# Kernel tuning notes

Hardware: AMD Instinct MI355X
Metric: run time of the kernel (lower is better)

The kernel has to match this reference:

```python
import jax, jax.numpy as jnp
import numpy as np

B, T, C, H = 8, 512, 1024, 16
N = C // H
DW, DA, DG = 64, 64, 128  # LoRA dims for decay / icl-rate / gate at C=1024

def _ln(x, w, b, eps=1e-5):
    mu = x.mean(-1, keepdims=True)
    var = ((x - mu) ** 2).mean(-1, keepdims=True)
    return (x - mu) * jax.lax.rsqrt(var + eps) * w + b

def _gn_heads(x, w, b, eps=64e-5):
    # GroupNorm(H groups) over channel dim of (B,T,C)
    xh = x.reshape(x.shape[0], x.shape[1], H, N)
    mu = xh.mean(-1, keepdims=True)
    var = ((xh - mu) ** 2).mean(-1, keepdims=True)
    xh = (xh - mu) * jax.lax.rsqrt(var + eps)
    return xh.reshape(x.shape) * w + b

def _shift(x):
    # RWKV time_shift: ZeroPad2d((0,0,1,-1))
    return jnp.concatenate([jnp.zeros_like(x[:, :1]), x[:, :-1]], axis=1)

def _wkv7(r, w_log, k, v, a, b):
    # all (B,T,H,N); state S (B,H,N,N): S = S*diag(exp(-exp(w))) + (S@a)b^T + v k^T; out = S@r
    decay = jnp.exp(-jnp.exp(w_log))
    def step(state, inp):
        r_t, d_t, k_t, v_t, a_t, b_t = inp
        sa = jnp.einsum('bhij,bhj->bhi', state, a_t)
        state = (state * d_t[:, :, None, :]
                 + sa[..., None] * b_t[:, :, None, :]
                 + v_t[..., None] * k_t[:, :, None, :])
        return state, jnp.einsum('bhij,bhj->bhi', state, r_t)
    xs = tuple(jnp.moveaxis(t, 1, 0) for t in (r, decay, k, v, a, b))
    s0 = jnp.zeros((r.shape[0], H, N, N), r.dtype)
    _, out = jax.lax.scan(step, s0, xs)
    return jnp.moveaxis(out, 0, 1)

def reference(x, v_first, ln_pre_w, ln_pre_b, ln_attn_w, ln_attn_b, ln_ffn_w, ln_ffn_b,
              x_r, x_w, x_k, x_v, x_a, x_g, w0, w1, w2, a0, a1, a2, g1, g2,
              k_k, k_a, r_k, W_r, W_k, W_v, W_o, gn_w, gn_b,
              ffn_x_k, W_ffn1, W_ffn2):
    Bx, Tx = x.shape[0], x.shape[1]
    x = _ln(x, ln_pre_w, ln_pre_b)            # pre_norm (layer_idx==0)
    # --- time mixing (RWKV7Attention) ---
    xn = _ln(x, ln_attn_w, ln_attn_b)
    dx = _shift(xn) - xn
    xr = xn + dx * x_r; xw = xn + dx * x_w; xk = xn + dx * x_k
    xv = xn + dx * x_v; xa = xn + dx * x_a; xg = xn + dx * x_g
    r = xr @ W_r
    w_log = -jax.nn.softplus(-(w0 + jnp.tanh(xw @ w1) @ w2)) - 0.5
    k = xk @ W_k
    v = xv @ W_v
    v_first = v                               # layer 0 stores v
    a = jax.nn.sigmoid(a0 + (xa @ a1) @ a2)   # in-context learning rate
    g = jax.nn.sigmoid(xg @ g1) @ g2          # gate
    kk = (k * k_k).reshape(Bx, Tx, H, N)
    kk = kk / jnp.maximum(jnp.linalg.norm(kk, axis=-1, keepdims=True), 1e-12)
    k = k * (1.0 + (a - 1.0) * k_a)
    rh = r.reshape(Bx, Tx, H, N)
    kh = k.reshape(Bx, Tx, H, N)
    vh = v.reshape(Bx, Tx, H, N)
    ah = a.reshape(Bx, Tx, H, N)
    o = _wkv7(rh, w_log.reshape(Bx, Tx, H, N), kh, vh, -kk, kk * ah)
    o = _gn_heads(o.reshape(Bx, Tx, C), gn_w, gn_b)
    o = o + ((rh * kh * r_k).sum(-1, keepdims=True) * vh).reshape(Bx, Tx, C)
    x = x + (o * g) @ W_o                     # residual (dropout p=0)
    # --- channel mixing (RWKV7FeedForward) ---
    xf = _ln(x, ln_ffn_w, ln_ffn_b)
    kf = xf + (_shift(xf) - xf) * ffn_x_k
    x = x + jnp.square(jax.nn.relu(kf @ W_ffn1)) @ W_ffn2
    return x, v_first

def setup_inputs() -> dict:
    key = jax.random.key(0)
    ks = iter(jax.random.split(key, 40))
    def nrm(shape, s=0.02):
        return jax.random.normal(next(ks), shape, jnp.float32) * s
    f32 = jnp.float32
    d = {
        'x': jax.random.normal(next(ks), (B, T, C), f32),
        'v_first': jnp.zeros((B, T, C), f32),
        'ln_pre_w': jnp.ones((C,), f32), 'ln_pre_b': jnp.zeros((C,), f32),
        'ln_attn_w': jnp.ones((C,), f32), 'ln_attn_b': jnp.zeros((C,), f32),
        'ln_ffn_w': jnp.ones((C,), f32), 'ln_ffn_b': jnp.zeros((C,), f32),
        'x_r': nrm((C,), 0.1), 'x_w': nrm((C,), 0.1), 'x_k': nrm((C,), 0.1),
        'x_v': nrm((C,), 0.1), 'x_a': nrm((C,), 0.1), 'x_g': nrm((C,), 0.1),
        'w0': nrm((C,), 0.5), 'w1': nrm((C, DW)), 'w2': nrm((DW, C)),
        'a0': nrm((C,), 0.1), 'a1': nrm((C, DA)), 'a2': nrm((DA, C)),
        'g1': nrm((C, DG)), 'g2': nrm((DG, C)),
        'k_k': 0.85 * jnp.ones((C,), f32) + nrm((C,), 0.05),
        'k_a': jnp.ones((C,), f32),
        'r_k': nrm((H, N), 0.1),
        'W_r': nrm((C, C)), 'W_k': nrm((C, C)), 'W_v': nrm((C, C)), 'W_o': nrm((C, C)),
        'gn_w': jnp.ones((C,), f32), 'gn_b': jnp.zeros((C,), f32),
        'ffn_x_k': nrm((C,), 0.1),
        'W_ffn1': nrm((C, 4 * C)), 'W_ffn2': nrm((4 * C, C)),
    }
    return d
```

## Files before the change

kernel.cpp:

```cpp
#include <hip/hip_runtime.h>

#define Bb 8
#define Tt 512
#define Cc 1024
#define Hh 16
#define Nh 64
#define Mm 4096
#define BTC 4194304
#define DEV __device__ __forceinline__

typedef __attribute__((ext_vector_type(8))) short short8;
typedef __attribute__((ext_vector_type(4))) float f32x4;

DEV unsigned short f2bf(float f) {
  unsigned int u = __builtin_bit_cast(unsigned int, f);
  u += 0x7fffu + ((u >> 16) & 1u);
  return (unsigned short)(u >> 16);
}

template <int CTRL>
DEV float dppadd(float x) {
  int xi = __builtin_bit_cast(int, x);
  int yi = __builtin_amdgcn_update_dpp(0, xi, CTRL, 0xF, 0xF, true);
  return x + __builtin_bit_cast(float, yi);
}

struct TDesc { const float* in; unsigned short* out; int K, N, bstart, nbx; };
struct TPack { TDesc d[12]; };

__global__ __launch_bounds__(256) void kt_transpose_multi(TPack p) {
  __shared__ float tile[32][33];
  const int bid = blockIdx.x;
  int i = 0;
  #pragma unroll
  for (int j = 1; j < 12; ++j) if (bid >= p.d[j].bstart) i = j;
  const float* in = p.d[i].in;
  unsigned short* out = p.d[i].out;
  const int K = p.d[i].K, N = p.d[i].N;
  const int local = bid - p.d[i].bstart;
  const int byq = local / p.d[i].nbx;
  const int bx = (local - byq * p.d[i].nbx) * 32;
  const int by = byq * 32;
  int tx = threadIdx.x, ty = threadIdx.y;
  #pragma unroll
  for (int q = ty; q < 32; q += 8) {
    int kk = by + q, nn = bx + tx;
    tile[q][tx] = (kk < K && nn < N) ? in[(size_t)kk * N + nn] : 0.f;
  }
  __syncthreads();
  #pragma unroll
  for (int q = ty; q < 32; q += 8) {
    int nn = bx + q, kk = by + tx;
    if (nn < N && kk < K) out[(size_t)nn * K + kk] = f2bf(tile[tx][q]);
  }
}

DEV void row_stats(float v0, float v1, float v2, float v3, float* red,
                   float& mu, float& rs, float eps) {
  float s = v0 + v1 + v2 + v3;
  float q = v0 * v0 + v1 * v1 + v2 * v2 + v3 * v3;
  #pragma unroll
  for (int o = 32; o; o >>= 1) { s += __shfl_down(s, o); q += __shfl_down(q, o); }
  int w = threadIdx.x >> 6;
  __syncthreads();
  if ((threadIdx.x & 63) == 0) { red[w] = s; red[4 + w] = q; }
  __syncthreads();
  s = red[0] + red[1] + red[2] + red[3];
  q = red[4] + red[5] + red[6] + red[7];
  mu = s * (1.f / 1024.f);
  float var = q * (1.f / 1024.f) - mu * mu;
  rs = rsqrtf(var + eps);
}

__global__ __launch_bounds__(256) void k1_mix(
    const float* __restrict__ x,
    const float* __restrict__ lnpw, const float* __restrict__ lnpb,
    const float* __restrict__ lnaw, const float* __restrict__ lnab,
    const float* __restrict__ cr, const float* __restrict__ cw,
    const float* __restrict__ ck, const float* __restrict__ cv,
    const float* __restrict__ ca, const float* __restrict__ cg,
    float* __restrict__ xln,
    unsigned short* __restrict__ mR, unsigned short* __restrict__ mW,
    unsigned short* __restrict__ mK, unsigned short* __restrict__ mV,
    unsigned short* __restrict__ mA, unsigned short* __restrict__ mG) {
  __shared__ float red[8];
  const int row = blockIdx.x;
  const int t = row & (Tt - 1);
  const int tid = threadIdx.x;
  const int c = tid * 4;
  const size_t base = (size_t)row * Cc + c;
  float a0 = x[base], a1 = x[base + 1], a2 = x[base + 2], a3 = x[base + 3];
  float mu, rs;
  row_stats(a0, a1, a2, a3, red, mu, rs, 1e-5f);
  float pw0 = lnpw[c], pw1 = lnpw[c + 1], pw2 = lnpw[c + 2], pw3 = lnpw[c + 3];
  float pb0 = lnpb[c], pb1 = lnpb[c + 1], pb2 = lnpb[c + 2], pb3 = lnpb[c + 3];
  float l0 = (a0 - mu) * rs * pw0 + pb0, l1 = (a1 - mu) * rs * pw1 + pb1;
  float l2 = (a2 - mu) * rs * pw2 + pb2, l3 = (a3 - mu) * rs * pw3 + pb3;
  float4 st; st.x = l0; st.y = l1; st.z = l2; st.w = l3;
  *(float4*)(xln + base) = st;
  row_stats(l0, l1, l2, l3, red, mu, rs, 1e-5f);
  float aw0 = lnaw[c], aw1 = lnaw[c + 1], aw2 = lnaw[c + 2], aw3 = lnaw[c + 3];
  float ab0 = lnab[c], ab1 = lnab[c + 1], ab2 = lnab[c + 2], ab3 = lnab[c + 3];
  float n0 = (l0 - mu) * rs * aw0 + ab0, n1 = (l1 - mu) * rs * aw1 + ab1;
  float n2 = (l2 - mu) * rs * aw2 + ab2, n3 = (l3 - mu) * rs * aw3 + ab3;
  float p0 = 0.f, p1 = 0.f, p2 = 0.f, p3 = 0.f;
  if (t > 0) {
    const size_t pb_ = base - Cc;
    float q0 = x[pb_], q1 = x[pb_ + 1], q2 = x[pb_ + 2], q3 = x[pb_ + 3];
    row_stats(q0, q1, q2, q3, red, mu, rs, 1e-5f);
    float e0 = (q0 - mu) * rs * pw0 + pb0, e1 = (q1 - mu) * rs * pw1 + pb1;
    float e2 = (q2 - mu) * rs * pw2 + pb2, e3 = (q3 - mu) * rs * pw3 + pb3;
    row_stats(e0, e1, e2, e3, red, mu, rs, 1e-5f);
    p0 = (e0 - mu) * rs * aw0 + ab0; p1 = (e1 - mu) * rs * aw1 + ab1;
    p2 = (e2 - mu) * rs * aw2 + ab2; p3 = (e3 - mu) * rs * aw3 + ab3;
  }
  float d0 = p0 - n0, d1 = p1 - n1, d2 = p2 - n2, d3 = p3 - n3;
  #define EMIT(cf, dst) { \
    float f0 = cf[c], f1 = cf[c + 1], f2 = cf[c + 2], f3 = cf[c + 3]; \
    ushort4 u; u.x = f2bf(n0 + d0 * f0); u.y = f2bf(n1 + d1 * f1); \
    u.z = f2bf(n2 + d2 * f2); u.w = f2bf(n3 + d3 * f3); \
    *(ushort4*)(dst + base) = u; }
  EMIT(cr, mR) EMIT(cw, mW) EMIT(ck, mK) EMIT(cv, mV) EMIT(ca, mA) EMIT(cg, mG)
  #undef EMIT
}

DEV void gll16(const unsigned short* g, unsigned short* l) {
  __builtin_amdgcn_global_load_lds(
      (const __attribute__((address_space(1))) void*)g,
      (__attribute__((address_space(3))) void*)l, 16, 0, 0);
}

template <int MODE>
DEV void gemm_epi(float z, size_t oi, int col,
                  float* outF, unsigned short* outB,
                  const float* bias, const float* res, float* outF2) {
  if constexpr (MODE == 0) outF[oi] = z;
  else if constexpr (MODE == 1) outB[oi] = f2bf(z);
  else if constexpr (MODE == 2) outB[oi] = f2bf(tanhf(z));
  else if constexpr (MODE == 3) outB[oi] = f2bf(1.f / (1.f + expf(-z)));
  else if constexpr (MODE == 4) { float m = fmaxf(z, 0.f); outB[oi] = f2bf(m * m); }
  else if constexpr (MODE == 5) { z += bias[col]; outF[oi] = 1.f / (1.f + expf(-z)); }
  else if constexpr (MODE == 6) {
    z += bias[col];
    float sg = 1.f / (1.f + expf(-z));
    outF[oi] = expf(-0.6065306597126334f * sg);
  } else if constexpr (MODE == 7) { outF[oi] = z + res[oi]; }
  else { float v = z + res[oi]; outF[oi] = v; outF2[oi] = v; }
}

DEV void gemm_epi_rt(int mode, float z, size_t oi, int col,
                     float* outF, unsigned short* outB, const float* bias) {
  if (mode == 0) outF[oi] = z;
  else if (mode == 1) outB[oi] = f2bf(z);
  else if (mode == 2) outB[oi] = f2bf(tanhf(z));
  else if (mode == 3) outB[oi] = f2bf(1.f / (1.f + expf(-z)));
  else if (mode == 5) { z += bias[col]; outF[oi] = 1.f / (1.f + expf(-z)); }
  else { z += bias[col]; float sg = 1.f / (1.f + expf(-z));
         outF[oi] = expf(-0.6065306597126334f * sg); }
}

template <int MODE>
__global__ __launch_bounds__(256) void kg_gemm64(
    const unsigned short* __restrict__ A, const unsigned short* __restrict__ Bt,
    int M, int Nn, int K,
    float* __restrict__ outF, unsigned short* __restrict__ outB,
    const float* __restrict__ bias, const float* __restrict__ res,
    float* __restrict__ outF2) {
  __shared__ unsigned short lsA[128 * 32];
  __shared__ unsigned short lsB[64 * 32];
  const int tid = threadIdx.x;
  const int lane = tid & 63;
  const int wave = tid >> 6;
  const int wy = wave >> 1, wx = wave & 1;
  const int m0 = blockIdx.y * 128;
  const int n0 = blockIdx.x * 64;
  const int sl4 = lane >> 2;
  const int sc = (lane & 3) << 3;
  f32x4 acc[4][2];
  #pragma unroll
  for (int i = 0; i < 4; ++i)
    #pragma unroll
    for (int j = 0; j < 2; ++j) { f32x4 z = {0.f, 0.f, 0.f, 0.f}; acc[i][j] = z; }
  const int fr = lane & 15;
  const int fk = (lane >> 4) << 3;
  for (int k0 = 0; k0 < K; k0 += 32) {
    #pragma unroll
    for (int j = 0; j < 2; ++j) {
      const int rb = (wave + j * 4) * 16;
      gll16(A + (size_t)(m0 + rb + sl4) * K + k0 + sc, lsA + rb * 32);
    }
    {
      const int rb = wave * 16;
      int br = n0 + rb + sl4;
      br = br < Nn ? br : Nn - 1;
      gll16(Bt + (size_t)br * K + k0 + sc, lsB + rb * 32);
    }
    __syncthreads();
    short8 af[4], bf[2];
    #pragma unroll
    for (int mt = 0; mt < 4; ++mt)
      af[mt] = *(const short8*)(lsA + (wy * 64 + mt * 16 + fr) * 32 + fk);
    #pragma unroll
    for (int nt = 0; nt < 2; ++nt)
      bf[nt] = *(const short8*)(lsB + (wx * 32 + nt * 16 + fr) * 32 + fk);
    #pragma unroll
    for (int mt = 0; mt < 4; ++mt)
      #pragma unroll
      for (int nt = 0; nt < 2; ++nt)
        acc[mt][nt] = __builtin_amdgcn_mfma_f32_16x16x32_bf16(af[mt], bf[nt], acc[mt][nt], 0, 0, 0);
    __syncthreads();
  }
  const int rbase = (lane >> 4) << 2;
  const int cbase = lane & 15;
  #pragma unroll
  for (int mt = 0; mt < 4; ++mt)
    #pragma unroll
    for (int nt = 0; nt < 2; ++nt)
      #pragma unroll
      for (int rr = 0; rr < 4; ++rr) {
        int row = m0 + wy * 64 + mt * 16 + rbase + rr;
        int col = n0 + wx * 32 + nt * 16 + cbase;
        if (col < Nn)
          gemm_epi<MODE>(acc[mt][nt][rr], (size_t)row * Nn + col, col, outF, outB, bias, res, outF2);
      }
}

DEV void gemm_body_rt(const unsigned short* A, const unsigned short* Bt,
                      int Nn, int K,
                      float* outF, unsigned short* outB, const float* bias,
                      unsigned short* lsA, unsigned short* lsB,
                      int m0, int n0, int mode) {
  const int tid = threadIdx.x;
  const int lane = tid & 63;
  const int wave = tid >> 6;
  const int wy = wave >> 1, wx = wave & 1;
  const int sl4 = lane >> 2;
  const int sc = (lane & 3) << 3;
  f32x4 acc[4][2];
  #pragma unroll
  for (int i = 0; i < 4; ++i)
    #pragma unroll
    for (int j = 0; j < 2; ++j) { f32x4 z = {0.f, 0.f, 0.f, 0.f}; acc[i][j] = z; }
  const int fr = lane & 15;
  const int fk = (lane >> 4) << 3;
  for (int k0 = 0; k0 < K; k0 += 32) {
    #pragma unroll
    for (int j = 0; j < 2; ++j) {
      const int rb = (wave + j * 4) * 16;
      gll16(A + (size_t)(m0 + rb + sl4) * K + k0 + sc, lsA + rb * 32);
    }
    {
      const int rb = wave * 16;
      int br = n0 + rb + sl4;
      br = br < Nn ? br : Nn - 1;
      gll16(Bt + (size_t)br * K + k0 + sc, lsB + rb * 32);
    }
    __syncthreads();
    short8 af[4], bf[2];
    #pragma unroll
    for (int mt = 0; mt < 4; ++mt)
      af[mt] = *(const short8*)(lsA + (wy * 64 + mt * 16 + fr) * 32 + fk);
    #pragma unroll
    for (int nt = 0; nt < 2; ++nt)
      bf[nt] = *(const short8*)(lsB + (wx * 32 + nt * 16 + fr) * 32 + fk);
    #pragma unroll
    for (int mt = 0; mt < 4; ++mt)
      #pragma unroll
      for (int nt = 0; nt < 2; ++nt)
        acc[mt][nt] = __builtin_amdgcn_mfma_f32_16x16x32_bf16(af[mt], bf[nt], acc[mt][nt], 0, 0, 0);
    __syncthreads();
  }
  const int rbase = (lane >> 4) << 2;
  const int cbase = lane & 15;
  #pragma unroll
  for (int mt = 0; mt < 4; ++mt)
    #pragma unroll
    for (int nt = 0; nt < 2; ++nt)
      #pragma unroll
      for (int rr = 0; rr < 4; ++rr) {
        int row = m0 + wy * 64 + mt * 16 + rbase + rr;
        int col = n0 + wx * 32 + nt * 16 + cbase;
        if (col < Nn)
          gemm_epi_rt(mode, acc[mt][nt][rr], (size_t)row * Nn + col, col, outF, outB, bias);
      }
}

__global__ __launch_bounds__(256) void kg_lora1(
    const unsigned short* __restrict__ mW, const unsigned short* __restrict__ mA,
    const unsigned short* __restrict__ mG,
    const unsigned short* __restrict__ w1T, const unsigned short* __restrict__ a1T,
    const unsigned short* __restrict__ g1T,
    unsigned short* __restrict__ tmpw, unsigned short* __restrict__ tmpa,
    unsigned short* __restrict__ tmpg) {
  __shared__ unsigned short lsA[128 * 32];
  __shared__ unsigned short lsB[64 * 32];
  const int z = blockIdx.z;
  const unsigned short* A  = z == 0 ? mW : z == 1 ? mA : mG;
  const unsigned short* Bt = z == 0 ? w1T : z == 1 ? a1T : g1T;
  unsigned short* outB     = z == 0 ? tmpw : z == 1 ? tmpa : tmpg;
  const int Nn = z < 2 ? 64 : 128;
  const int n0 = z < 2 ? 0 : (z - 2) * 64;
  const int mode = z == 0 ? 2 : z == 1 ? 1 : 3;
  gemm_body_rt(A, Bt, Nn, 1024, nullptr, outB, nullptr, lsA, lsB,
               blockIdx.y * 128, n0, mode);
}

__global__ __launch_bounds__(256) void kg_lora2(
    const unsigned short* __restrict__ tmpw, const unsigned short* __restrict__ tmpa,
    const unsigned short* __restrict__ tmpg,
    const unsigned short* __restrict__ w2T, const unsigned short* __restrict__ a2T,
    const unsigned short* __restrict__ g2T,
    float* __restrict__ decay, float* __restrict__ aicl, float* __restrict__ gout,
    const float* __restrict__ w0v, const float* __restrict__ a0v) {
  __shared__ unsigned short lsA[128 * 32];
  __shared__ unsigned short lsB[64 * 32];
  const int z = blockIdx.z;
  const unsigned short* A  = z == 0 ? tmpw : z == 1 ? tmpa : tmpg;
  const unsigned short* Bt = z == 0 ? w2T : z == 1 ? a2T : g2T;
  float* outF              = z == 0 ? decay : z == 1 ? aicl : gout;
  const float* bias        = z == 0 ? w0v : z == 1 ? a0v : nullptr;
  const int K = z < 2 ? 64 : 128;
  const int mode = z == 0 ? 6 : z == 1 ? 5 : 0;
  gemm_body_rt(A, Bt, 1024, K, outF, nullptr, bias, lsA, lsB,
               blockIdx.y * 128, blockIdx.x * 64, mode);
}

template <int MODE>
__global__ __launch_bounds__(512, 1) void kg_gemm8p(
    const unsigned short* __restrict__ A, const unsigned short* __restrict__ Bt,
    int Nn, int Kstride, int Klen,
    float* __restrict__ outF, unsigned short* __restrict__ outB) {
  __shared__ unsigned short lds[3 * 24576];
  const int tid = threadIdx.x;
  const int lane = tid & 63;
  const int wave = tid >> 6;
  const int wm = wave >> 2, wn = wave & 3;
  const int m0 = blockIdx.y * 128;
  const int n0 = blockIdx.x * 256;
  const int kbase = blockIdx.z * Klen;
  const int ntile = Klen / 64;
  const int fr = lane & 15;
  const int fkb = (lane >> 4) << 4;

  int arow[2], acolb[2], brow[4], bcolb[4];
  #pragma unroll
  for (int i = 0; i < 2; ++i) {
    int off = i * 8192 + tid * 16;
    int r = off >> 7;
    arow[i] = r; acolb[i] = (off & 127) ^ ((r & 7) << 4);
  }
  #pragma unroll
  for (int i = 0; i < 4; ++i) {
    int off = i * 8192 + tid * 16;
    int r = off >> 7;
    brow[i] = r; bcolb[i] = (off & 127) ^ ((r & 7) << 4);
  }

  #define STAGE(t_) { \
    int tc = (t_) < ntile ? (t_) : ntile - 1; \
    unsigned short* lb_ = lds + ((t_) % 3) * 24576; \
    const int kk = kbase + tc * 64; \
    _Pragma("unroll") \
    for (int i = 0; i < 2; ++i) \
      gll16(A + (size_t)(m0 + arow[i]) * Kstride + kk + (acolb[i] >> 1), \
            lb_ + i * 4096 + wave * 512); \
    _Pragma("unroll") \
    for (int i = 0; i < 4; ++i) \
      gll16(Bt + (size_t)(n0 + brow[i]) * Kstride + kk + (bcolb[i] >> 1), \
            lb_ + 8192 + i * 4096 + wave * 512); \
  }

  f32x4 acc[4][4];
  #pragma unroll
  for (int i = 0; i < 4; ++i)
    #pragma unroll
    for (int j = 0; j < 4; ++j) { f32x4 z = {0.f, 0.f, 0.f, 0.f}; acc[i][j] = z; }

  STAGE(0)
  STAGE(1)
  asm volatile("s_waitcnt vmcnt(6)" ::: "memory");
  __syncthreads();

  for (int t = 0; t < ntile; ++t) {
    STAGE(t + 2)
    const unsigned short* lb = lds + (t % 3) * 24576;
    #pragma unroll
    for (int ks = 0; ks < 2; ++ks) {
      short8 af[4], bf[4];
      #pragma unroll
      for (int mt = 0; mt < 4; ++mt) {
        int r = wm * 64 + mt * 16 + fr;
        int byt = (ks * 64 + fkb) ^ ((r & 7) << 4);
        af[mt] = *(const short8*)(lb + r * 64 + (byt >> 1));
      }
      #pragma unroll
      for (int nt = 0; nt < 4; ++nt) {
        int r = wn * 64 + nt * 16 + fr;
        int byt = (ks * 64 + fkb) ^ ((r & 7) << 4);
        bf[nt] = *(const short8*)(lb + 8192 + r * 64 + (byt >> 1));
      }
      __builtin_amdgcn_s_setprio(1);
      #pragma unroll
      for (int mt = 0; mt < 4; ++mt)
        #pragma unroll
        for (int nt = 0; nt < 4; ++nt)
          acc[mt][nt] = __builtin_amdgcn_mfma_f32_16x16x32_bf16(af[mt], bf[nt], acc[mt][nt], 0, 0, 0);
      __builtin_amdgcn_s_setprio(0);
    }
    asm volatile("s_waitcnt vmcnt(6)" ::: "memory");
    __syncthreads();
  }
  #undef STAGE

  const int rbase = (lane >> 4) << 2;
  const int cbase = lane & 15;
  #pragma unroll
  for (int mt = 0; mt < 4; ++mt)
    #pragma unroll
    for (int nt = 0; nt < 4; ++nt)
      #pragma unroll
      for (int rr = 0; rr < 4; ++rr) {
        int row = m0 + wm * 64 + mt * 16 + rbase + rr;
        int col = n0 + wn * 64 + nt * 16 + cbase;
        size_t oi = (size_t)row * Nn + col;
        float z = acc[mt][nt][rr];
        if constexpr (MODE == 4) { float m = fmaxf(z, 0.f); outB[oi] = f2bf(m * m); }
        else atomicAdd(outF + oi, z);
      }
}

__global__ __launch_bounds__(256) void kg_qkv_fused(
    const unsigned short* __restrict__ A0, const unsigned short* __restrict__ A1,
    const unsigned short* __restrict__ A2,
    const unsigned short* __restrict__ B0, const unsigned short* __restrict__ B1,
    const unsigned short* __restrict__ B2,
    float* __restrict__ rbuf, float* __restrict__ kbuf, float* __restrict__ vout,
    const float* __restrict__ aicl,
    const float* __restrict__ kkc, const float* __restrict__ kac,
    float* __restrict__ awb, float* __restrict__ bwb) {
  __shared__ unsigned short lsA[128 * 32];
  __shared__ unsigned short lsB[128 * 32];
  const int z = blockIdx.z;
  const unsigned short* A = z == 0 ? A0 : z == 1 ? A1 : A2;
  const unsigned short* Bt = z == 0 ? B0 : z == 1 ? B1 : B2;
  const int tid = threadIdx.x;
  const int lane = tid & 63;
  const int wave = tid >> 6;
  const int wy = wave >> 1, wx = wave & 1;
  const int m0 = blockIdx.y * 128;
  const int n0 = blockIdx.x * 128;
  const int sl4 = lane >> 2;
  const int sc = (lane & 3) << 3;
  f32x4 acc[4][4];
  #pragma unroll
  for (int i = 0; i < 4; ++i)
    #pragma unroll
    for (int j = 0; j < 4; ++j) { f32x4 zz = {0.f, 0.f, 0.f, 0.f}; acc[i][j] = zz; }
  const int fr = lane & 15;
  const int fk = (lane >> 4) << 3;
  for (int k0 = 0; k0 < 1024; k0 += 32) {
    #pragma unroll
    for (int j = 0; j < 2; ++j) {
      const int rb = (wave + j * 4) * 16;
      gll16(A + (size_t)(m0 + rb + sl4) * 1024 + k0 + sc, lsA + rb * 32);
      gll16(Bt + (size_t)(n0 + rb + sl4) * 1024 + k0 + sc, lsB + rb * 32);
    }
    __syncthreads();
    short8 af[4], bf[4];
    #pragma unroll
    for (int mt = 0; mt < 4; ++mt)
      af[mt] = *(const short8*)(lsA + (wy * 64 + mt * 16 + fr) * 32 + fk);
    #pragma unroll
    for (int nt = 0; nt < 4; ++nt)
      bf[nt] = *(const short8*)(lsB + (wx * 64 + nt * 16 + fr) * 32 + fk);
    #pragma unroll
    for (int mt = 0; mt < 4; ++mt)
      #pragma unroll
      for (int nt = 0; nt < 4; ++nt)
        acc[mt][nt] = __builtin_amdgcn_mfma_f32_16x16x32_bf16(af[mt], bf[nt], acc[mt][nt], 0, 0, 0);
    __syncthreads();
  }
  const int rbase = (lane >> 4) << 2;
  const int cbase = lane & 15;
  if (z != 1) {
    float* outF = z == 0 ? rbuf : vout;
    #pragma unroll
    for (int mt = 0; mt < 4; ++mt)
      #pragma unroll
      for (int nt = 0; nt < 4; ++nt)
        #pragma unroll
        for (int rr = 0; rr < 4; ++rr) {
          int row = m0 + wy * 64 + mt * 16 + rbase + rr;
          int col = n0 + wx * 64 + nt * 16 + cbase;
          outF[(size_t)row * Cc + col] = acc[mt][nt][rr];
        }
  } else {
    float kkc4[4], kac4[4];
    #pragma unroll
    for (int nt = 0; nt < 4; ++nt) {
      int col = n0 + wx * 64 + nt * 16 + cbase;
      kkc4[nt] = kkc[col];
      kac4[nt] = kac[col];
    }
    #pragma unroll
    for (int mt = 0; mt < 4; ++mt)
      #pragma unroll
      for (int rr = 0; rr < 4; ++rr) {
        int row = m0 + wy * 64 + mt * 16 + rbase + rr;
        float h0 = acc[mt][0][rr] * kkc4[0];
        float h1 = acc[mt][1][rr] * kkc4[1];
        float h2 = acc[mt][2][rr] * kkc4[2];
        float h3 = acc[mt][3][rr] * kkc4[3];
        float ss = (h0 * h0 + h1 * h1) + (h2 * h2 + h3 * h3);
        ss = dppadd<0xB1>(ss);
        ss = dppadd<0x4E>(ss);
        ss = dppadd<0x124>(ss);
        ss = dppadd<0x128>(ss);
        float inv = 1.f / fmaxf(sqrtf(ss), 1e-12f);
        #pragma unroll
        for (int nt = 0; nt < 4; ++nt) {
          int col = n0 + wx * 64 + nt * 16 + cbase;
          size_t oi = (size_t)row * Cc + col;
          float kv = acc[mt][nt][rr];
          float hn = kv * kkc4[nt] * inv;
          float av = aicl[oi];
          awb[oi] = -hn;
          bwb[oi] = hn * av;
          kbuf[oi] = kv * (1.f + (av - 1.f) * kac4[nt]);
        }
      }
  }
}

#define CS 8
__global__ __launch_bounds__(512, 2) void k5_wkv7(
    const float* __restrict__ r, const float* __restrict__ dec,
    const float* __restrict__ k, const float* __restrict__ v,
    const float* __restrict__ aw, const float* __restrict__ bw,
    float* __restrict__ o) {
  const int blk = blockIdx.x;
  const int bh = blk & 127, half = blk >> 7;
  const int b = bh >> 4, h = bh & 15;
  const int tid = threadIdx.x;
  const int lane = tid & 63;
  const int w = tid >> 6;
  const int cg = lane & 15;
  const int rw = lane >> 4;
  const int row = half * 32 + w * 4 + rw;
  const int cb = cg << 2;

  __shared__ float buf[2][6 * CS * 64];

  float S[4];
  #pragma unroll
  for (int j = 0; j < 4; ++j) S[j] = 0.f;

  const size_t base = (size_t)b * Tt * Cc + (size_t)h * Nh;

  const float* sptr = w == 0 ? aw : w == 1 ? dec : w == 2 ? bw
                    : w == 3 ? k  : w == 4 ? r   : v;
  const int srow = lane >> 4;
  const int scol = (lane & 15) << 2;

  uint4 R0, R1;
  #define LOADC(cstart) if (w < 6) { \
    const size_t g0 = base + (size_t)((cstart) + srow) * Cc + scol; \
    R0 = *(const uint4*)(sptr + g0); \
    R1 = *(const uint4*)(sptr + g0 + 4 * Cc); }

  LOADC(0)

  #pragma unroll 1
  for (int c = 0; c < Tt / CS; ++c) {
    float* bp = buf[c & 1];
    if (w < 6) {
      *(uint4*)(bp + w * 512 + (lane << 2)) = R0;
      *(uint4*)(bp + w * 512 + 256 + (lane << 2)) = R1;
    }
    const int cn = (c + 1 < Tt / CS) ? (c + 1) : c;
    LOADC(cn * CS)
    __syncthreads();

    float4 Aq[2], Dq[2], Bq[2], Kq[2], Rq[2];
    float Vv[2];
    #define LOADOPS(slot, ss) { \
      const float* sp_ = bp + (ss) * 64; \
      Aq[slot] = *(const float4*)(sp_ + cb); \
      Dq[slot] = *(const float4*)(sp_ + 512 + cb); \
      Bq[slot] = *(const float4*)(sp_ + 1024 + cb); \
      Kq[slot] = *(const float4*)(sp_ + 1536 + cb); \
      Rq[slot] = *(const float4*)(sp_ + 2048 + cb); \
      Vv[slot] = sp_[2560 + row]; }

    LOADOPS(0, 0)
    #pragma unroll
    for (int s = 0; s < CS; ++s) {
      const int cu = s & 1, nx = cu ^ 1;
      if (s + 1 < CS) LOADOPS(nx, s + 1)

      float4 a4 = Aq[cu];
      float sa = fmaf(S[1], a4.y, S[0] * a4.x) + fmaf(S[3], a4.w, S[2] * a4.z);
      sa = dppadd<0xB1>(sa);
      sa = dppadd<0x4E>(sa);
      sa = dppadd<0x124>(sa);
      sa = dppadd<0x128>(sa);

      const float vv = Vv[cu];
      float4 d4 = Dq[cu], b4 = Bq[cu], k4 = Kq[cu], r4 = Rq[cu];
      S[0] = fmaf(S[0], d4.x, fmaf(vv, k4.x, sa * b4.x));
      float oo = S[0] * r4.x;
      S[1] = fmaf(S[1], d4.y, fmaf(vv, k4.y, sa * b4.y));
      oo = fmaf(S[1], r4.y, oo);
      S[2] = fmaf(S[2], d4.z, fmaf(vv, k4.z, sa * b4.z));
      oo = fmaf(S[2], r4.z, oo);
      S[3] = fmaf(S[3], d4.w, fmaf(vv, k4.w, sa * b4.w));
      oo = fmaf(S[3], r4.w, oo);

      oo = dppadd<0xB1>(oo);
      oo = dppadd<0x4E>(oo);
      oo = dppadd<0x124>(oo);
      oo = dppadd<0x128>(oo);
      if (cg == 0) o[base + (size_t)(c * CS + s) * Cc + row] = oo;
    }
    #undef LOADOPS
  }
  #undef LOADC
}

__global__ __launch_bounds__(256) void k6_out(
    const float* __restrict__ o, const float* __restrict__ r, const float* __restrict__ k,
    const float* __restrict__ v, const float* __restrict__ rk,
    const float* __restrict__ gnw, const float* __restrict__ gnb,
    const float* __restrict__ g, unsigned short* __restrict__ og) {
  const int row = blockIdx.x, tid = threadIdx.x;
  const int c = tid * 4;
  const size_t base = (size_t)row * Cc + c;
  float o0 = o[base], o1 = o[base + 1], o2 = o[base + 2], o3 = o[base + 3];
  float r0 = r[base], r1 = r[base + 1], r2 = r[base + 2], r3 = r[base + 3];
  float k0 = k[base], k1 = k[base + 1], k2 = k[base + 2], k3 = k[base + 3];
  float s = o0 + o1 + o2 + o3;
  float q = o0 * o0 + o1 * o1 + o2 * o2 + o3 * o3;
  float bs = r0 * k0 * rk[c] + r1 * k1 * rk[c + 1] + r2 * k2 * rk[c + 2] + r3 * k3 * rk[c + 3];
  #pragma unroll
  for (int m = 8; m; m >>= 1) {
    s += __shfl_xor(s, m); q += __shfl_xor(q, m); bs += __shfl_xor(bs, m);
  }
  float mu = s * (1.f / 64.f);
  float var = q * (1.f / 64.f) - mu * mu;
  float rs = rsqrtf(var + 64e-5f);
  float v0 = v[base], v1 = v[base + 1], v2 = v[base + 2], v3 = v[base + 3];
  float z0 = (o0 - mu) * rs * gnw[c] + gnb[c] + bs * v0;
  float z1 = (o1 - mu) * rs * gnw[c + 1] + gnb[c + 1] + bs * v1;
  float z2 = (o2 - mu) * rs * gnw[c + 2] + gnb[c + 2] + bs * v2;
  float z3 = (o3 - mu) * rs * gnw[c + 3] + gnb[c + 3] + bs * v3;
  ushort4 u;
  u.x = f2bf(z0 * g[base]); u.y = f2bf(z1 * g[base + 1]);
  u.z = f2bf(z2 * g[base + 2]); u.w = f2bf(z3 * g[base + 3]);
  *(ushort4*)(og + base) = u;
}

__global__ __launch_bounds__(256) void k8_ffnmix(
    const float* __restrict__ x2, const float* __restrict__ lnw, const float* __restrict__ lnb,
    const float* __restrict__ fxk, unsigned short* __restrict__ kf) {
  __shared__ float red[8];
  const int row = blockIdx.x;
  const int t = row & (Tt - 1);
  const int tid = threadIdx.x;
  const int c = tid * 4;
  const size_t base = (size_t)row * Cc + c;
  float a0 = x2[base], a1 = x2[base + 1], a2 = x2[base + 2], a3 = x2[base + 3];
  float mu, rs;
  row_stats(a0, a1, a2, a3, red, mu, rs, 1e-5f);
  float w0 = lnw[c], w1 = lnw[c + 1], w2 = lnw[c + 2], w3 = lnw[c + 3];
  float b0 = lnb[c], b1 = lnb[c + 1], b2 = lnb[c + 2], b3 = lnb[c + 3];
  float f0 = (a0 - mu) * rs * w0 + b0, f1 = (a1 - mu) * rs * w1 + b1;
  float f2 = (a2 - mu) * rs * w2 + b2, f3 = (a3 - mu) * rs * w3 + b3;
  float p0 = 0.f, p1 = 0.f, p2 = 0.f, p3 = 0.f;
  if (t > 0) {
    const size_t pb_ = base - Cc;
    float q0 = x2[pb_], q1 = x2[pb_ + 1], q2 = x2[pb_ + 2], q3 = x2[pb_ + 3];
    row_stats(q0, q1, q2, q3, red, mu, rs, 1e-5f);
    p0 = (q0 - mu) * rs * w0 + b0; p1 = (q1 - mu) * rs * w1 + b1;
    p2 = (q2 - mu) * rs * w2 + b2; p3 = (q3 - mu) * rs * w3 + b3;
  }
  ushort4 u;
  u.x = f2bf(f0 + (p0 - f0) * fxk[c]);
  u.y = f2bf(f1 + (p1 - f1) * fxk[c + 1]);
  u.z = f2bf(f2 + (p2 - f2) * fxk[c + 2]);
  u.w = f2bf(f3 + (p3 - f3) * fxk[c + 3]);
  *(ushort4*)(kf + base) = u;
}

extern "C" void kernel_launch(void* const* d_in, const int* in_sizes, int n_in,
                              void* d_out, int out_size, void* d_ws, size_t ws_size,
                              hipStream_t stream) {
  (void)in_sizes; (void)n_in; (void)out_size; (void)ws_size;
  const float* x    = (const float*)d_in[0];
  const float* lnpw = (const float*)d_in[2];
  const float* lnpb = (const float*)d_in[3];
  const float* lnaw = (const float*)d_in[4];
  const float* lnab = (const float*)d_in[5];
  const float* lnfw = (const float*)d_in[6];
  const float* lnfb = (const float*)d_in[7];
  const float* cxr  = (const float*)d_in[8];
  const float* cxw  = (const float*)d_in[9];
  const float* cxk  = (const float*)d_in[10];
  const float* cxv  = (const float*)d_in[11];
  const float* cxa  = (const float*)d_in[12];
  const float* cxg  = (const float*)d_in[13];
  const float* w0v  = (const float*)d_in[14];
  const float* w1m  = (const float*)d_in[15];
  const float* w2m  = (const float*)d_in[16];
  const float* a0v  = (const float*)d_in[17];
  const float* a1m  = (const float*)d_in[18];
  const float* a2m  = (const float*)d_in[19];
  const float* g1m  = (const float*)d_in[20];
  const float* g2m  = (const float*)d_in[21];
  const float* kkv  = (const float*)d_in[22];
  const float* kav  = (const float*)d_in[23];
  const float* rkv  = (const float*)d_in[24];
  const float* Wr   = (const float*)d_in[25];
  const float* Wk   = (const float*)d_in[26];
  const float* Wv   = (const float*)d_in[27];
  const float* Wo   = (const float*)d_in[28];
  const float* gnw  = (const float*)d_in[29];
  const float* gnb  = (const float*)d_in[30];
  const float* fxk  = (const float*)d_in[31];
  const float* Wf1  = (const float*)d_in[32];
  const float* Wf2  = (const float*)d_in[33];

  char* ws = (char*)d_ws;
  float* outx = (float*)d_out;
  float* vout = outx + BTC;

  size_t off = 0;
  unsigned short* WrT  = (unsigned short*)(ws + off); off += 2097152;
  unsigned short* WkT  = (unsigned short*)(ws + off); off += 2097152;
  unsigned short* WvT  = (unsigned short*)(ws + off); off += 2097152;
  unsigned short* WoT  = (unsigned short*)(ws + off); off += 2097152;
  unsigned short* Wf1T = (unsigned short*)(ws + off); off += 8388608;
  unsigned short* Wf2T = (unsigned short*)(ws + off); off += 8388608;
  unsigned short* w1T  = (unsigned short*)(ws + off); off += 131072;
  unsigned short* w2T  = (unsigned short*)(ws + off); off += 131072;
  unsigned short* a1T  = (unsigned short*)(ws + off); off += 131072;
  unsigned short* a2T  = (unsigned short*)(ws + off); off += 131072;
  unsigned short* g1T  = (unsigned short*)(ws + off); off += 262144;
  unsigned short* g2T  = (unsigned short*)(ws + off); off += 262144;
  float* xln = (float*)(ws + off); off += 16777216;
  unsigned short* mixR = (unsigned short*)(ws + off);
  unsigned short* mixW = (unsigned short*)(ws + off + 8388608);
  unsigned short* mixK = (unsigned short*)(ws + off + 16777216);
  unsigned short* mixV = (unsigned short*)(ws + off + 25165824);
  unsigned short* mixA = (unsigned short*)(ws + off + 33554432);
  unsigned short* mixG = (unsigned short*)(ws + off + 41943040);
  unsigned short* hbuf = (unsigned short*)(ws + off);
  off += 50331648;
  unsigned short* tmpw = (unsigned short*)(ws + off); off += 524288;
  unsigned short* tmpa = (unsigned short*)(ws + off); off += 524288;
  unsigned short* tmpg = (unsigned short*)(ws + off); off += 1048576;
  float* decay = (float*)(ws + off);
  unsigned short* og = (unsigned short*)(ws + off);
  off += 16777216;
  float* aicl = (float*)(ws + off);
  float* obuf = (float*)(ws + off);
  off += 16777216;
  float* gout = (float*)(ws + off); off += 16777216;
  float* rbuf = (float*)(ws + off);
  float* x2   = (float*)(ws + off);
  off += 16777216;
  float* kbuf = (float*)(ws + off); off += 16777216;
  float* awb  = (float*)(ws + off);
  unsigned short* kf = (unsigned short*)(ws + off);
  off += 16777216;
  float* bwb  = (float*)(ws + off); off += 16777216;

  dim3 tb(32, 8);
  TPack tp;
  tp.d[0]  = TDesc{Wr,  WrT,  1024, 1024, 0,     32};
  tp.d[1]  = TDesc{Wk,  WkT,  1024, 1024, 1024,  32};
  tp.d[2]  = TDesc{Wv,  WvT,  1024, 1024, 2048,  32};
  tp.d[3]  = TDesc{Wo,  WoT,  1024, 1024, 3072,  32};
  tp.d[4]  = TDesc{Wf1, Wf1T, 1024, 4096, 4096,  128};
  tp.d[5]  = TDesc{Wf2, Wf2T, 4096, 1024, 8192,  32};
  tp.d[6]  = TDesc{w1m, w1T,  1024, 64,   12288, 2};
  tp.d[7]  = TDesc{w2m, w2T,  64,   1024, 12352, 32};
  tp.d[8]  = TDesc{a1m, a1T,  1024, 64,   12416, 2};
  tp.d[9]  = TDesc{a2m, a2T,  64,   1024, 12480, 32};
  tp.d[10] = TDesc{g1m, g1T,  1024, 128,  12544, 4};
  tp.d[11] = TDesc{g2m, g2T,  128,  1024, 12672, 32};
  kt_transpose_multi<<<12800, tb, 0, stream>>>(tp);

  k1_mix<<<Mm, 256, 0, stream>>>(x, lnpw, lnpb, lnaw, lnab, cxr, cxw, cxk, cxv, cxa, cxg,
                                 xln, mixR, mixW, mixK, mixV, mixA, mixG);

  kg_lora1<<<dim3(1, 32, 4), 256, 0, stream>>>(mixW, mixA, mixG, w1T, a1T, g1T,
                                               tmpw, tmpa, tmpg);
  kg_lora2<<<dim3(16, 32, 3), 256, 0, stream>>>(tmpw, tmpa, tmpg, w2T, a2T, g2T,
                                                decay, aicl, gout, w0v, a0v);

  kg_qkv_fused<<<dim3(8, 32, 3), 256, 0, stream>>>(mixR, mixK, mixV, WrT, WkT, WvT,
                                                   rbuf, kbuf, vout,
                                                   aicl, kkv, kav, awb, bwb);

  k5_wkv7<<<256, 512, 0, stream>>>(rbuf, decay, kbuf, vout, awb, bwb, obuf);
  k6_out<<<Mm, 256, 0, stream>>>(obuf, rbuf, kbuf, vout, rkv, gnw, gnb, gout, og);
  kg_gemm64<9><<<dim3(16, 32), 256, 0, stream>>>(og, WoT, Mm, 1024, 1024, x2, nullptr, nullptr, xln, outx);
  k8_ffnmix<<<Mm, 256, 0, stream>>>(x2, lnfw, lnfb, fxk, kf);
  kg_gemm8p<4><<<dim3(16, 32, 1), 512, 0, stream>>>(kf, Wf1T, 4096, 1024, 1024, nullptr, hbuf);
  kg_gemm8p<8><<<dim3(4, 32, 2), 512, 0, stream>>>(hbuf, Wf2T, 1024, 4096, 2048, outx, nullptr);
}
```

Measured before the change: 572.6 us.

## Rewrite QKV GEMM with 8-wave 128x256 tiles and triple-buffered swizzled LDS

Replaces the fused R/K/V projection GEMM's single-buffered 128x128 tile loop (K-step 32, two syncs per step) with an 8-wave 128x256 tile that uses K-step 64. Global-to-LDS loads run through a three-stage ring with vmcnt-based waits, and the LDS layout is XOR-swizzled to avoid bank conflicts. MFMA sections are raised in priority. The goal is to overlap global loads with MFMA work and cut sync overhead, at the cost of about 144KB of LDS per block, one block per CU, and fewer blocks (384) in the grid.

```diff
diff --git a/kernel.cpp b/kernel.cpp
--- a/kernel.cpp
+++ b/kernel.cpp
@@ -429,7 +429,7 @@
       }
 }
 
-__global__ __launch_bounds__(256) void kg_qkv_fused(
+__global__ __launch_bounds__(512, 1) void kg_qkv8p(
     const unsigned short* __restrict__ A0, const unsigned short* __restrict__ A1,
     const unsigned short* __restrict__ A2,
     const unsigned short* __restrict__ B0, const unsigned short* __restrict__ B1,
@@ -438,48 +438,90 @@
     const float* __restrict__ aicl,
     const float* __restrict__ kkc, const float* __restrict__ kac,
     float* __restrict__ awb, float* __restrict__ bwb) {
-  __shared__ unsigned short lsA[128 * 32];
-  __shared__ unsigned short lsB[128 * 32];
+  __shared__ unsigned short lds[3 * 24576];
   const int z = blockIdx.z;
-  const unsigned short* A = z == 0 ? A0 : z == 1 ? A1 : A2;
+  const unsigned short* A  = z == 0 ? A0 : z == 1 ? A1 : A2;
   const unsigned short* Bt = z == 0 ? B0 : z == 1 ? B1 : B2;
   const int tid = threadIdx.x;
   const int lane = tid & 63;
   const int wave = tid >> 6;
-  const int wy = wave >> 1, wx = wave & 1;
+  const int wm = wave >> 2, wn = wave & 3;
   const int m0 = blockIdx.y * 128;
-  const int n0 = blockIdx.x * 128;
-  const int sl4 = lane >> 2;
-  const int sc = (lane & 3) << 3;
+  const int n0 = blockIdx.x * 256;
+  const int ntile = 16;
+  const int fr = lane & 15;
+  const int fkb = (lane >> 4) << 4;
+
+  int arow[2], acolb[2], brow[4], bcolb[4];
+  #pragma unroll
+  for (int i = 0; i < 2; ++i) {
+    int off = i * 8192 + tid * 16;
+    int r = off >> 7;
+    arow[i] = r; acolb[i] = (off & 127) ^ ((r & 7) << 4);
+  }
+  #pragma unroll
+  for (int i = 0; i < 4; ++i) {
+    int off = i * 8192 + tid * 16;
+    int r = off >> 7;
+    brow[i] = r; bcolb[i] = (off & 127) ^ ((r & 7) << 4);
+  }
+
+  #define STAGE(t_) { \
+    int tc = (t_) < ntile ? (t_) : ntile - 1; \
+    unsigned short* lb_ = lds + ((t_) % 3) * 24576; \
+    const int kk = tc * 64; \
+    _Pragma("unroll") \
+    for (int i = 0; i < 2; ++i) \
+      gll16(A + (size_t)(m0 + arow[i]) * 1024 + kk + (acolb[i] >> 1), \
+            lb_ + i * 4096 + wave * 512); \
+    _Pragma("unroll") \
+    for (int i = 0; i < 4; ++i) \
+      gll16(Bt + (size_t)(n0 + brow[i]) * 1024 + kk + (bcolb[i] >> 1), \
+            lb_ + 8192 + i * 4096 + wave * 512); \
+  }
+
   f32x4 acc[4][4];
   #pragma unroll
   for (int i = 0; i < 4; ++i)
     #pragma unroll
     for (int j = 0; j < 4; ++j) { f32x4 zz = {0.f, 0.f, 0.f, 0.f}; acc[i][j] = zz; }
-  const int fr = lane & 15;
-  const int fk = (lane >> 4) << 3;
-  for (int k0 = 0; k0 < 1024; k0 += 32) {
-    #pragma unroll
-    for (int j = 0; j < 2; ++j) {
-      const int rb = (wave + j * 4) * 16;
-      gll16(A + (size_t)(m0 + rb + sl4) * 1024 + k0 + sc, lsA + rb * 32);
-      gll16(Bt + (size_t)(n0 + rb + sl4) * 1024 + k0 + sc, lsB + rb * 32);
+
+  STAGE(0)
+  STAGE(1)
+  asm volatile("s_waitcnt vmcnt(6)" ::: "memory");
+  __syncthreads();
+
+  for (int t = 0; t < ntile; ++t) {
+    STAGE(t + 2)
+    const unsigned short* lb = lds + (t % 3) * 24576;
+    #pragma unroll
+    for (int ks = 0; ks < 2; ++ks) {
+      short8 af[4], bf[4];
+      #pragma unroll
+      for (int mt = 0; mt < 4; ++mt) {
+        int r = wm * 64 + mt * 16 + fr;
+        int byt = (ks * 64 + fkb) ^ ((r & 7) << 4);
+        af[mt] = *(const short8*)(lb + r * 64 + (byt >> 1));
+      }
+      #pragma unroll
+      for (int nt = 0; nt < 4; ++nt) {
+        int r = wn * 64 + nt * 16 + fr;
+        int byt = (ks * 64 + fkb) ^ ((r & 7) << 4);
+        bf[nt] = *(const short8*)(lb + 8192 + r * 64 + (byt >> 1));
+      }
+      __builtin_amdgcn_s_setprio(1);
+      #pragma unroll
+      for (int mt = 0; mt < 4; ++mt)
+        #pragma unroll
+        for (int nt = 0; nt < 4; ++nt)
+          acc[mt][nt] = __builtin_amdgcn_mfma_f32_16x16x32_bf16(af[mt], bf[nt], acc[mt][nt], 0, 0, 0);
+      __builtin_amdgcn_s_setprio(0);
     }
+    asm volatile("s_waitcnt vmcnt(6)" ::: "memory");
     __syncthreads();
-    short8 af[4], bf[4];
-    #pragma unroll
-    for (int mt = 0; mt < 4; ++mt)
-      af[mt] = *(const short8*)(lsA + (wy * 64 + mt * 16 + fr) * 32 + fk);
-    #pragma unroll
-    for (int nt = 0; nt < 4; ++nt)
-      bf[nt] = *(const short8*)(lsB + (wx * 64 + nt * 16 + fr) * 32 + fk);
-    #pragma unroll
-    for (int mt = 0; mt < 4; ++mt)
-      #pragma unroll
-      for (int nt = 0; nt < 4; ++nt)
-        acc[mt][nt] = __builtin_amdgcn_mfma_f32_16x16x32_bf16(af[mt], bf[nt], acc[mt][nt], 0, 0, 0);
-    __syncthreads();
-  }
+  }
+  #undef STAGE
+
   const int rbase = (lane >> 4) << 2;
   const int cbase = lane & 15;
   if (z != 1) {
@@ -490,15 +532,15 @@
       for (int nt = 0; nt < 4; ++nt)
         #pragma unroll
         for (int rr = 0; rr < 4; ++rr) {
-          int row = m0 + wy * 64 + mt * 16 + rbase + rr;
-          int col = n0 + wx * 64 + nt * 16 + cbase;
+          int row = m0 + wm * 64 + mt * 16 + rbase + rr;
+          int col = n0 + wn * 64 + nt * 16 + cbase;
           outF[(size_t)row * Cc + col] = acc[mt][nt][rr];
         }
   } else {
     float kkc4[4], kac4[4];
     #pragma unroll
     for (int nt = 0; nt < 4; ++nt) {
-      int col = n0 + wx * 64 + nt * 16 + cbase;
+      int col = n0 + wn * 64 + nt * 16 + cbase;
       kkc4[nt] = kkc[col];
       kac4[nt] = kac[col];
     }
@@ -506,7 +548,7 @@
     for (int mt = 0; mt < 4; ++mt)
       #pragma unroll
       for (int rr = 0; rr < 4; ++rr) {
-        int row = m0 + wy * 64 + mt * 16 + rbase + rr;
+        int row = m0 + wm * 64 + mt * 16 + rbase + rr;
         float h0 = acc[mt][0][rr] * kkc4[0];
         float h1 = acc[mt][1][rr] * kkc4[1];
         float h2 = acc[mt][2][rr] * kkc4[2];
@@ -519,7 +561,7 @@
         float inv = 1.f / fmaxf(sqrtf(ss), 1e-12f);
         #pragma unroll
         for (int nt = 0; nt < 4; ++nt) {
-          int col = n0 + wx * 64 + nt * 16 + cbase;
+          int col = n0 + wn * 64 + nt * 16 + cbase;
           size_t oi = (size_t)row * Cc + col;
           float kv = acc[mt][nt][rr];
           float hn = kv * kkc4[nt] * inv;
@@ -798,9 +840,9 @@
   kg_lora2<<<dim3(16, 32, 3), 256, 0, stream>>>(tmpw, tmpa, tmpg, w2T, a2T, g2T,
                                                 decay, aicl, gout, w0v, a0v);
 
-  kg_qkv_fused<<<dim3(8, 32, 3), 256, 0, stream>>>(mixR, mixK, mixV, WrT, WkT, WvT,
-                                                   rbuf, kbuf, vout,
-                                                   aicl, kkv, kav, awb, bwb);
+  kg_qkv8p<<<dim3(4, 32, 3), 512, 0, stream>>>(mixR, mixK, mixV, WrT, WkT, WvT,
+                                               rbuf, kbuf, vout,
+                                               aicl, kkv, kav, awb, bwb);
 
   k5_wkv7<<<256, 512, 0, stream>>>(rbuf, decay, kbuf, vout, awb, bwb, obuf);
   k6_out<<<Mm, 256, 0, stream>>>(obuf, rbuf, kbuf, vout, rkv, gnw, gnb, gout, og);
```

Result: faster. 556.4 us (-2.8%).
